# Performance work log

Hardware: AMD Instinct MI355X
Metric: run time of the kernel (lower is better)

Reference implementation:

```python
import jax, jax.numpy as jnp
import numpy as np

EPS = 1e-5

def layer_norm(x, w, b):
    mu = jnp.mean(x, axis=-1, keepdims=True)
    var = jnp.var(x, axis=-1, keepdims=True)
    return (x - mu) / jnp.sqrt(var + EPS) * w + b

def setup_inputs() -> dict:
    key = jax.random.key(0)
    B, N, C = 4, 4096, 1024
    H = 16
    MW = 4 * C
    ks = jax.random.split(key, 8)
    s = 0.02
    return {
        "x": jax.random.normal(ks[0], (B, N, C), dtype=jnp.float32),
        "ln1_w": jnp.ones((C,), jnp.float32), "ln1_b": jnp.zeros((C,), jnp.float32),
        "q_w": jax.random.normal(ks[1], (C, C), jnp.float32) * s, "q_b": jnp.zeros((C,), jnp.float32),
        "k_w": jax.random.normal(ks[2], (C, C), jnp.float32) * s, "k_b": jnp.zeros((C,), jnp.float32),
        "v_w": jax.random.normal(ks[3], (C, C), jnp.float32) * s, "v_b": jnp.zeros((C,), jnp.float32),
        "o_w": jax.random.normal(ks[4], (C, C), jnp.float32) * s, "o_b": jnp.zeros((C,), jnp.float32),
        "ln2_w": jnp.ones((C,), jnp.float32), "ln2_b": jnp.zeros((C,), jnp.float32),
        "fc_w": jax.random.normal(ks[5], (MW, C), jnp.float32) * s, "fc_b": jnp.zeros((MW,), jnp.float32),
        "proj_w": jax.random.normal(ks[6], (C, MW), jnp.float32) * s, "proj_b": jnp.zeros((C,), jnp.float32),
    }

def reference(x, ln1_w, ln1_b, q_w, q_b, k_w, k_b, v_w, v_b, o_w, o_b,
              ln2_w, ln2_b, fc_w, fc_b, proj_w, proj_b):
    B, N, C = x.shape
    H = 16
    D = C // H
    xn = layer_norm(x, ln1_w, ln1_b)
    # projections, reshape to (B, N, H, D), transpose to (B, H, N, D)
    q = (xn @ q_w.T + q_b).reshape(B, N, H, D).transpose(0, 2, 1, 3)
    k = (xn @ k_w.T + k_b).reshape(B, N, H, D).transpose(0, 2, 1, 3)
    v = (xn @ v_w.T + v_b).reshape(B, N, H, D).transpose(0, 2, 1, 3)
    # faithful to original: einsum labels treat the HEAD axis as contraction axis
    q = jax.nn.elu(q) + 1.0
    k = jax.nn.elu(k) + 1.0
    kv = jnp.einsum('bhnd,bhne->bnde', k, v)            # sum over heads -> (B,N,D,D)
    qkv = jnp.einsum('bhnd,bnde->bhne', q, kv)          # (B,H,N,D)
    k_sum = k.sum(axis=1)                               # sum over heads -> (B,N,D)
    qk = jnp.einsum('bhnd,bnd->bhn', q, k_sum)          # (B,H,N)
    attn = qkv / qk[..., None]                          # (B,H,N,D)
    attn = attn.transpose(0, 2, 1, 3).reshape(B, N, C)
    attn = attn @ o_w.T + o_b
    x = x + attn
    xn2 = layer_norm(x, ln2_w, ln2_b)
    h = jax.nn.gelu(xn2 @ fc_w.T + fc_b, approximate=False)
    x = x + (h @ proj_w.T + proj_b)
    return x
```

## Files before the change

### kernel.cpp

```cpp
#include <hip/hip_runtime.h>
#include <math.h>

typedef unsigned short u16;
typedef unsigned int   u32;
typedef __attribute__((ext_vector_type(8))) short bf16x8;
typedef __attribute__((ext_vector_type(4))) float f32x4;
typedef __attribute__((ext_vector_type(4))) unsigned short u16x4;

__device__ __forceinline__ float bf2f(u16 v){ return __uint_as_float(((u32)v) << 16); }
__device__ __forceinline__ u16 f2bf(float f){
  u32 u = __float_as_uint(f);
  return (u16)((u + 0x7fffu + ((u >> 16) & 1u)) >> 16);
}
__device__ __forceinline__ float elu1(float x){ return x > 0.f ? x + 1.f : __expf(x); }
__device__ __forceinline__ float gelu_f(float v){
  float u = 0.7978845608f * (v + 0.044715f * v * v * v);
  float e = __expf(-2.f * fabsf(u));
  float th = copysignf((1.f - e) / (1.f + e), u);
  return 0.5f * v * (1.f + th);
}

__global__ __launch_bounds__(256) void k_cast(const float* __restrict__ src, u16* __restrict__ dst, int n4){
  int i = blockIdx.x * 256 + threadIdx.x;
  int stride = gridDim.x * 256;
  for (; i < n4; i += stride){
    float4 v = ((const float4*)src)[i];
    u16x4 o; o.x = f2bf(v.x); o.y = f2bf(v.y); o.z = f2bf(v.z); o.w = f2bf(v.w);
    ((u16x4*)dst)[i] = o;
  }
}

__global__ void k_cat3(const float* __restrict__ a, const float* __restrict__ b,
                       const float* __restrict__ c, float* __restrict__ dst){
  int i = blockIdx.x * 256 + threadIdx.x;
  dst[i] = i < 1024 ? a[i] : (i < 2048 ? b[i - 1024] : c[i - 2048]);
}

__global__ __launch_bounds__(256) void k_ln(const float* __restrict__ x, const float* __restrict__ w,
                                            const float* __restrict__ b, u16* __restrict__ out){
  const int t = threadIdx.x;
  const size_t m = blockIdx.x;
  float4 v = ((const float4*)(x + m * 1024))[t];
  float s  = v.x + v.y + v.z + v.w;
  float s2 = v.x*v.x + v.y*v.y + v.z*v.z + v.w*v.w;
  #pragma unroll
  for (int o = 32; o > 0; o >>= 1){ s += __shfl_down(s, o, 64); s2 += __shfl_down(s2, o, 64); }
  __shared__ float red[8];
  if ((t & 63) == 0){ red[t >> 6] = s; red[4 + (t >> 6)] = s2; }
  __syncthreads();
  s  = red[0] + red[1] + red[2] + red[3];
  s2 = red[4] + red[5] + red[6] + red[7];
  float mu  = s * (1.f / 1024.f);
  float inv = rsqrtf(s2 * (1.f / 1024.f) - mu * mu + 1e-5f);
  float4 wv = ((const float4*)w)[t];
  float4 bv = ((const float4*)b)[t];
  u16x4 o;
  o.x = f2bf((v.x - mu) * inv * wv.x + bv.x);
  o.y = f2bf((v.y - mu) * inv * wv.y + bv.y);
  o.z = f2bf((v.z - mu) * inv * wv.z + bv.z);
  o.w = f2bf((v.w - mu) * inv * wv.w + bv.w);
  ((u16x4*)(out + m * 1024))[t] = o;
}

__global__ __launch_bounds__(256) void k_attn(const u16* __restrict__ qkv, u16* __restrict__ out){
  __shared__ float qe[4][16][68];
  __shared__ float ke[4][16][68];
  __shared__ float sm[4][16][20];
  const int w = threadIdx.x >> 6, lane = threadIdx.x & 63;
  const size_t m = (size_t)blockIdx.x * 4 + w;
  const u16* base = qkv + m * 3072;
  #pragma unroll
  for (int i = 0; i < 8; ++i){
    int idx = i * 64 + lane;
    int h = idx >> 5, c2 = (idx & 31) * 2;
    u32 qv = ((const u32*)base)[idx];
    u32 kv = ((const u32*)base)[512 + idx];
    float2 qf, kf;
    qf.x = elu1(bf2f((u16)(qv & 0xffffu))); qf.y = elu1(bf2f((u16)(qv >> 16)));
    kf.x = elu1(bf2f((u16)(kv & 0xffffu))); kf.y = elu1(bf2f((u16)(kv >> 16)));
    *(float2*)&qe[w][h][c2] = qf;
    *(float2*)&ke[w][h][c2] = kf;
  }
  float vr[16];
  #pragma unroll
  for (int h = 0; h < 16; ++h) vr[h] = bf2f(base[2048 + h * 64 + lane]);
  __syncthreads();
  const int sh = lane >> 2, jb = lane & 3;
  float sacc[4] = {0.f, 0.f, 0.f, 0.f};
  #pragma unroll
  for (int d4 = 0; d4 < 16; ++d4){
    float4 q4 = *(const float4*)&qe[w][sh][d4 * 4];
    #pragma unroll
    for (int j = 0; j < 4; ++j){
      float4 k4 = *(const float4*)&ke[w][4 * jb + j][d4 * 4];
      sacc[j] += q4.x*k4.x + q4.y*k4.y + q4.z*k4.z + q4.w*k4.w;
    }
  }
  #pragma unroll
  for (int j = 0; j < 4; ++j) sm[w][sh][4 * jb + j] = sacc[j];
  float part = sacc[0] + sacc[1] + sacc[2] + sacc[3];
  part += __shfl_xor(part, 1, 64);
  part += __shfl_xor(part, 2, 64);
  if (jb == 0) sm[w][sh][16] = part;
  __syncthreads();
  float acc[16];
  #pragma unroll
  for (int h = 0; h < 16; ++h) acc[h] = 0.f;
  #pragma unroll
  for (int h = 0; h < 16; ++h){
    #pragma unroll
    for (int j4 = 0; j4 < 4; ++j4){
      float4 s4 = *(const float4*)&sm[w][h][j4 * 4];
      acc[h] += s4.x*vr[4*j4] + s4.y*vr[4*j4+1] + s4.z*vr[4*j4+2] + s4.w*vr[4*j4+3];
    }
  }
  u16* ob = out + m * 1024;
  #pragma unroll
  for (int h = 0; h < 16; ++h)
    ob[h * 64 + lane] = f2bf(acc[h] / sm[w][h][16]);
}

template<int Q, int IB, int AE>
__device__ __forceinline__ void quadf(f32x4 (&acc)[8][4], bf16x8 (&a)[AE][2], bf16x8 (&b)[4][2]){
  __builtin_amdgcn_s_setprio(1);
  #pragma unroll
  for (int s = 0; s < 2; ++s)
    #pragma unroll
    for (int i = 0; i < 2; ++i)
      #pragma unroll
      for (int nf = 0; nf < 4; ++nf)
        acc[2*Q+i][nf] = __builtin_amdgcn_mfma_f32_16x16x32_bf16(a[IB+i][s], b[nf][s], acc[2*Q+i][nf], 0, 0, 0);
  __builtin_amdgcn_s_setprio(0);
}

template<int EPI>
__global__ __launch_bounds__(512, 2) void k_gemm(const u16* __restrict__ A, const u16* __restrict__ W,
                                                 const float* __restrict__ bias, const float* __restrict__ res,
                                                 void* __restrict__ outp, int N, int K, int nbn){
  __shared__ alignas(16) char lds[131072];
  const int tid  = threadIdx.x;
  const int lane = tid & 63, wid = tid >> 6;
  const int wr = wid >> 2, wc = wid & 3;
  const int g = lane >> 4, l15 = lane & 15;
  const int nwg = gridDim.x, bid = blockIdx.x;
  const int swz = (bid & 7) * (nwg >> 3) + (bid >> 3);
  const int m0 = (swz / nbn) * 256, n0 = (swz % nbn) * 256;
  const u16* gA = A + (size_t)m0 * K;
  const u16* gW = W + (size_t)n0 * K;
  const int nt = K >> 6;

  f32x4 acc[8][4];
  #pragma unroll
  for (int i = 0; i < 8; ++i)
    #pragma unroll
    for (int j = 0; j < 4; ++j) acc[i][j] = (f32x4){0.f, 0.f, 0.f, 0.f};

  auto stageA = [&](int b, int kt, int h){
    char* dst = lds + b * 65536 + h * 16384 + wid * 1024;
    const u16* src = gA + (size_t)(h * 128) * K + (kt << 6);
    #pragma unroll
    for (int i = 0; i < 2; ++i){
      int li = i * 512 + tid;
      int r  = li >> 3;
      int ch = (li & 7) ^ (r & 7);
      __builtin_amdgcn_global_load_lds(
        (const __attribute__((address_space(1))) u32*)(src + (size_t)r * K + ch * 8),
        (__attribute__((address_space(3))) u32*)(dst + i * 8192), 16, 0, 0);
    }
  };
  auto stageB = [&](int b, int kt, int h){
    char* dst = lds + b * 65536 + 32768 + h * 16384 + wid * 1024;
    const u16* src = gW + (size_t)(h * 128) * K + (kt << 6);
    #pragma unroll
    for (int i = 0; i < 2; ++i){
      int li = i * 512 + tid;
      int r  = li >> 3;
      int ch = (li & 7) ^ (r & 7);
      __builtin_amdgcn_global_load_lds(
        (const __attribute__((address_space(1))) u32*)(src + (size_t)r * K + ch * 8),
        (__attribute__((address_space(3))) u32*)(dst + i * 8192), 16, 0, 0);
    }
  };

  stageA(0, 0, 0); stageA(0, 0, 1); stageB(0, 0, 0); stageB(0, 0, 1);
  if (nt > 1){
    stageA(1, 1, 0); stageA(1, 1, 1);
    asm volatile("s_waitcnt vmcnt(4)" ::: "memory");
  } else {
    asm volatile("s_waitcnt vmcnt(0)" ::: "memory");
  }
  __builtin_amdgcn_s_barrier();

  for (int t = 0; t < nt; ++t){
    const int c = t & 1;
    const char* Ab = lds + c * 65536;
    const char* Bb = Ab + 32768;
    bf16x8 bfr[4][2], aQ[2][2], aH[4][2];

    #pragma unroll
    for (int nf = 0; nf < 4; ++nf)
      #pragma unroll
      for (int s = 0; s < 2; ++s){
        int row = wc * 64 + nf * 16 + l15;
        bfr[nf][s] = *(const bf16x8*)(Bb + row * 128 + (((4 * s + g) ^ (row & 7)) << 4));
      }
    #pragma unroll
    for (int i = 0; i < 2; ++i)
      #pragma unroll
      for (int s = 0; s < 2; ++s){
        int row = wr * 128 + i * 16 + l15;
        aQ[i][s] = *(const bf16x8*)(Ab + row * 128 + (((4 * s + g) ^ (row & 7)) << 4));
      }
    if (t + 1 < nt) stageB(c ^ 1, t + 1, 0);
    __builtin_amdgcn_s_barrier();
    quadf<0, 0>(acc, aQ, bfr);
    __builtin_amdgcn_s_barrier();

    #pragma unroll
    for (int i = 0; i < 2; ++i)
      #pragma unroll
      for (int s = 0; s < 2; ++s){
        int row = wr * 128 + (2 + i) * 16 + l15;
        aQ[i][s] = *(const bf16x8*)(Ab + row * 128 + (((4 * s + g) ^ (row & 7)) << 4));
      }
    #pragma unroll
    for (int i = 0; i < 4; ++i)
      #pragma unroll
      for (int s = 0; s < 2; ++s){
        int row = wr * 128 + (4 + i) * 16 + l15;
        aH[i][s] = *(const bf16x8*)(Ab + row * 128 + (((4 * s + g) ^ (row & 7)) << 4));
      }
    if (t + 1 < nt) stageB(c ^ 1, t + 1, 1);
    __builtin_amdgcn_s_barrier();
    quadf<1, 0>(acc, aQ, bfr);
    asm volatile("s_waitcnt lgkmcnt(0)" ::: "memory");
    __builtin_amdgcn_s_barrier();

    if (t + 2 < nt) stageA(c, t + 2, 0);
    __builtin_amdgcn_s_barrier();
    quadf<2, 0>(acc, aH, bfr);
    __builtin_amdgcn_s_barrier();

    if (t + 2 < nt){
      stageA(c, t + 2, 1);
      asm volatile("s_waitcnt vmcnt(4)" ::: "memory");
    } else {
      asm volatile("s_waitcnt vmcnt(0)" ::: "memory");
    }
    __builtin_amdgcn_s_barrier();
    quadf<3, 2>(acc, aH, bfr);
    __builtin_amdgcn_s_barrier();
  }

  #pragma unroll
  for (int mf = 0; mf < 8; ++mf){
    #pragma unroll
    for (int nf = 0; nf < 4; ++nf){
      int row = m0 + wr * 128 + mf * 16 + 4 * g;
      int col = n0 + wc * 64 + nf * 16 + l15;
      float bcol = bias[col];
      #pragma unroll
      for (int r = 0; r < 4; ++r){
        float v = acc[mf][nf][r] + bcol;
        size_t idx = (size_t)(row + r) * N + col;
        if constexpr (EPI == 0){
          ((u16*)outp)[idx] = f2bf(v);
        } else if constexpr (EPI == 1){
          ((float*)outp)[idx] = res[idx] + v;
        } else if constexpr (EPI == 2){
          ((u16*)outp)[idx] = f2bf(gelu_f(v));
        } else {
          float* o = (float*)outp; o[idx] = o[idx] + v;
        }
      }
    }
  }
}

extern "C" void kernel_launch(void* const* d_in, const int* in_sizes, int n_in,
                              void* d_out, int out_size, void* d_ws, size_t ws_size,
                              hipStream_t stream){
  (void)in_sizes; (void)n_in; (void)out_size; (void)ws_size;
  const float* x    = (const float*)d_in[0];
  const float* ln1w = (const float*)d_in[1];
  const float* ln1b = (const float*)d_in[2];
  const float* qw   = (const float*)d_in[3];
  const float* qb   = (const float*)d_in[4];
  const float* kw   = (const float*)d_in[5];
  const float* kb   = (const float*)d_in[6];
  const float* vw   = (const float*)d_in[7];
  const float* vb   = (const float*)d_in[8];
  const float* ow   = (const float*)d_in[9];
  const float* ob   = (const float*)d_in[10];
  const float* ln2w = (const float*)d_in[11];
  const float* ln2b = (const float*)d_in[12];
  const float* fcw  = (const float*)d_in[13];
  const float* fcb  = (const float*)d_in[14];
  const float* pw   = (const float*)d_in[15];
  const float* pb   = (const float*)d_in[16];

  char* ws = (char*)d_ws;
  u16*   WQKV = (u16*)(ws + 0);
  u16*   WO   = (u16*)(ws + 6291456);
  u16*   WFC  = (u16*)(ws + 8388608);
  u16*   WPR  = (u16*)(ws + 16777216);
  float* BQ   = (float*)(ws + 25165824);
  u16*   XN   = (u16*)(ws + 25178112);
  u16*   QKV  = (u16*)(ws + 58732544);
  u16*   ATT  = (u16*)(ws + 159395840);
  u16*   H    = QKV;
  float* OUT  = (float*)d_out;

  k_cast<<<512, 256, 0, stream>>>(qw, WQKV,           262144);
  k_cast<<<512, 256, 0, stream>>>(kw, WQKV + 1048576, 262144);
  k_cast<<<512, 256, 0, stream>>>(vw, WQKV + 2097152, 262144);
  k_cast<<<512, 256, 0, stream>>>(ow, WO,             262144);
  k_cast<<<1024, 256, 0, stream>>>(fcw, WFC,          1048576);
  k_cast<<<1024, 256, 0, stream>>>(pw,  WPR,          1048576);
  k_cat3<<<12, 256, 0, stream>>>(qb, kb, vb, BQ);

  k_ln<<<16384, 256, 0, stream>>>(x, ln1w, ln1b, XN);
  k_gemm<0><<<64 * 12, 512, 0, stream>>>(XN, WQKV, BQ, nullptr, QKV, 3072, 1024, 12);
  k_attn<<<4096, 256, 0, stream>>>(QKV, ATT);
  k_gemm<1><<<64 * 4, 512, 0, stream>>>(ATT, WO, ob, x, OUT, 1024, 1024, 4);

  k_ln<<<16384, 256, 0, stream>>>(OUT, ln2w, ln2b, XN);
  k_gemm<2><<<64 * 16, 512, 0, stream>>>(XN, WFC, fcb, nullptr, H, 4096, 1024, 16);
  k_gemm<3><<<64 * 4, 512, 0, stream>>>(H, WPR, pb, nullptr, OUT, 1024, 4096, 4);
}
```

Measured before the change: 571.6 us.

## Software-pipeline LDS fragment reads in GEMM main loop with double-buffered registers

Restructures the GEMM K-loop so each quarter's A fragments are read from LDS while the previous quarter's MFMAs run. Both A and B register fragments are now double-buffered, and the next tile's B fragments and first A quarter are prefetched before the last MFMA quarter. The loop is unrolled by two so buffer indices are compile-time constants. Barriers per iteration drop from eight to about two, which cuts synchronization stalls. The extra register buffers raise VGPR pressure at 512 threads with two blocks per CU, and the loop assumes nt is even or handled by the t+1 guards.

```diff
diff --git a/kernel.cpp b/kernel.cpp
--- a/kernel.cpp
+++ b/kernel.cpp
@@ -120,8 +120,8 @@
     ob[h * 64 + lane] = f2bf(acc[h] / sm[w][h][16]);
 }
 
-template<int Q, int IB, int AE>
-__device__ __forceinline__ void quadf(f32x4 (&acc)[8][4], bf16x8 (&a)[AE][2], bf16x8 (&b)[4][2]){
+template<int Q>
+__device__ __forceinline__ void quadf(f32x4 (&acc)[8][4], const bf16x8 (&a)[2][2], const bf16x8 (&b)[4][2]){
   __builtin_amdgcn_s_setprio(1);
   #pragma unroll
   for (int s = 0; s < 2; ++s)
@@ -129,7 +129,7 @@
     for (int i = 0; i < 2; ++i)
       #pragma unroll
       for (int nf = 0; nf < 4; ++nf)
-        acc[2*Q+i][nf] = __builtin_amdgcn_mfma_f32_16x16x32_bf16(a[IB+i][s], b[nf][s], acc[2*Q+i][nf], 0, 0, 0);
+        acc[2*Q+i][nf] = __builtin_amdgcn_mfma_f32_16x16x32_bf16(a[i][s], b[nf][s], acc[2*Q+i][nf], 0, 0, 0);
   __builtin_amdgcn_s_setprio(0);
 }
 
@@ -181,6 +181,27 @@
         (__attribute__((address_space(3))) u32*)(dst + i * 8192), 16, 0, 0);
     }
   };
+  auto rdA = [&](bf16x8 (&d)[2][2], const char* Abase, int q){
+    #pragma unroll
+    for (int i = 0; i < 2; ++i)
+      #pragma unroll
+      for (int s = 0; s < 2; ++s){
+        int row = wr * 128 + (2 * q + i) * 16 + l15;
+        d[i][s] = *(const bf16x8*)(Abase + row * 128 + (((4 * s + g) ^ (row & 7)) << 4));
+      }
+  };
+  auto rdB = [&](bf16x8 (&d)[4][2], const char* Bbase){
+    #pragma unroll
+    for (int nf = 0; nf < 4; ++nf)
+      #pragma unroll
+      for (int s = 0; s < 2; ++s){
+        int row = wc * 64 + nf * 16 + l15;
+        d[nf][s] = *(const bf16x8*)(Bbase + row * 128 + (((4 * s + g) ^ (row & 7)) << 4));
+      }
+  };
+
+  bf16x8 bfr[2][4][2];
+  bf16x8 aQ[2][2][2];
 
   stageA(0, 0, 0); stageA(0, 0, 1); stageB(0, 0, 0); stageB(0, 0, 1);
   if (nt > 1){
@@ -190,66 +211,39 @@
     asm volatile("s_waitcnt vmcnt(0)" ::: "memory");
   }
   __builtin_amdgcn_s_barrier();
-
-  for (int t = 0; t < nt; ++t){
-    const int c = t & 1;
-    const char* Ab = lds + c * 65536;
-    const char* Bb = Ab + 32768;
-    bf16x8 bfr[4][2], aQ[2][2], aH[4][2];
-
-    #pragma unroll
-    for (int nf = 0; nf < 4; ++nf)
-      #pragma unroll
-      for (int s = 0; s < 2; ++s){
-        int row = wc * 64 + nf * 16 + l15;
-        bfr[nf][s] = *(const bf16x8*)(Bb + row * 128 + (((4 * s + g) ^ (row & 7)) << 4));
-      }
-    #pragma unroll
-    for (int i = 0; i < 2; ++i)
-      #pragma unroll
-      for (int s = 0; s < 2; ++s){
-        int row = wr * 128 + i * 16 + l15;
-        aQ[i][s] = *(const bf16x8*)(Ab + row * 128 + (((4 * s + g) ^ (row & 7)) << 4));
-      }
-    if (t + 1 < nt) stageB(c ^ 1, t + 1, 0);
-    __builtin_amdgcn_s_barrier();
-    quadf<0, 0>(acc, aQ, bfr);
-    __builtin_amdgcn_s_barrier();
-
-    #pragma unroll
-    for (int i = 0; i < 2; ++i)
-      #pragma unroll
-      for (int s = 0; s < 2; ++s){
-        int row = wr * 128 + (2 + i) * 16 + l15;
-        aQ[i][s] = *(const bf16x8*)(Ab + row * 128 + (((4 * s + g) ^ (row & 7)) << 4));
-      }
-    #pragma unroll
-    for (int i = 0; i < 4; ++i)
-      #pragma unroll
-      for (int s = 0; s < 2; ++s){
-        int row = wr * 128 + (4 + i) * 16 + l15;
-        aH[i][s] = *(const bf16x8*)(Ab + row * 128 + (((4 * s + g) ^ (row & 7)) << 4));
-      }
-    if (t + 1 < nt) stageB(c ^ 1, t + 1, 1);
-    __builtin_amdgcn_s_barrier();
-    quadf<1, 0>(acc, aQ, bfr);
-    asm volatile("s_waitcnt lgkmcnt(0)" ::: "memory");
-    __builtin_amdgcn_s_barrier();
-
-    if (t + 2 < nt) stageA(c, t + 2, 0);
-    __builtin_amdgcn_s_barrier();
-    quadf<2, 0>(acc, aH, bfr);
-    __builtin_amdgcn_s_barrier();
-
-    if (t + 2 < nt){
-      stageA(c, t + 2, 1);
-      asm volatile("s_waitcnt vmcnt(4)" ::: "memory");
-    } else {
-      asm volatile("s_waitcnt vmcnt(0)" ::: "memory");
-    }
-    __builtin_amdgcn_s_barrier();
-    quadf<3, 2>(acc, aH, bfr);
-    __builtin_amdgcn_s_barrier();
+  rdB(bfr[0], lds + 32768);
+  rdA(aQ[0], lds, 0);
+
+  for (int t0 = 0; t0 < nt; t0 += 2){
+    #pragma unroll
+    for (int u = 0; u < 2; ++u){
+      const int t = t0 + u;
+      const char* Ab  = lds + u * 65536;
+      const char* Bb1 = lds + (u ^ 1) * 65536 + 32768;
+      const char* Ab1 = lds + (u ^ 1) * 65536;
+      if (t + 1 < nt) stageB(u ^ 1, t + 1, 0);
+      rdA(aQ[1], Ab, 1);
+      quadf<0>(acc, aQ[0], bfr[u]);
+      if (t + 1 < nt) stageB(u ^ 1, t + 1, 1);
+      rdA(aQ[0], Ab, 2);
+      quadf<1>(acc, aQ[1], bfr[u]);
+      rdA(aQ[1], Ab, 3);
+      quadf<2>(acc, aQ[0], bfr[u]);
+      asm volatile("s_waitcnt lgkmcnt(0)" ::: "memory");
+      __builtin_amdgcn_s_barrier();
+      if (t + 2 < nt){
+        stageA(u, t + 2, 0); stageA(u, t + 2, 1);
+        asm volatile("s_waitcnt vmcnt(4)" ::: "memory");
+      } else if (t + 1 < nt){
+        asm volatile("s_waitcnt vmcnt(0)" ::: "memory");
+      }
+      if (t + 1 < nt){
+        __builtin_amdgcn_s_barrier();
+        rdB(bfr[u ^ 1], Bb1);
+        rdA(aQ[0], Ab1, 0);
+      }
+      quadf<3>(acc, aQ[1], bfr[u]);
+    }
   }
 
   #pragma unroll
```

After: 852.7 us. +49.2%, slower.

## Restructure GEMM main loop into 4x2 MFMA quadrants with reduced register fragments

Applied to the files above, without the earlier changes.

Each k-step of the GEMM main loop now runs as four quadrants of 4 M-fragments by 2 N-fragments instead of four phases of 2 M-fragments by 4 N-fragments. LDS fragment reads are interleaved differently: B halves are loaded in two parts and A halves are reused across both B halves. Both A stagings for t+2 are issued together. The aim is to cut live register fragments and rebalance LDS reads against MFMA work, but the extra lgkmcnt waits before each quadrant may expose LDS latency.

```diff
diff --git a/kernel.cpp b/kernel.cpp
--- a/kernel.cpp
+++ b/kernel.cpp
@@ -120,16 +120,16 @@
     ob[h * 64 + lane] = f2bf(acc[h] / sm[w][h][16]);
 }
 
-template<int Q, int IB, int AE>
-__device__ __forceinline__ void quadf(f32x4 (&acc)[8][4], bf16x8 (&a)[AE][2], bf16x8 (&b)[4][2]){
+template<int QM, int QN>
+__device__ __forceinline__ void quad16(f32x4 (&acc)[8][4], const bf16x8 (&a)[4][2], const bf16x8 (&b)[2][2]){
   __builtin_amdgcn_s_setprio(1);
   #pragma unroll
   for (int s = 0; s < 2; ++s)
     #pragma unroll
-    for (int i = 0; i < 2; ++i)
+    for (int i = 0; i < 4; ++i)
       #pragma unroll
-      for (int nf = 0; nf < 4; ++nf)
-        acc[2*Q+i][nf] = __builtin_amdgcn_mfma_f32_16x16x32_bf16(a[IB+i][s], b[nf][s], acc[2*Q+i][nf], 0, 0, 0);
+      for (int j = 0; j < 2; ++j)
+        acc[QM*4+i][QN*2+j] = __builtin_amdgcn_mfma_f32_16x16x32_bf16(a[i][s], b[j][s], acc[QM*4+i][QN*2+j], 0, 0, 0);
   __builtin_amdgcn_s_setprio(0);
 }
 
@@ -181,6 +181,27 @@
         (__attribute__((address_space(3))) u32*)(dst + i * 8192), 16, 0, 0);
     }
   };
+  auto rdA4 = [&](bf16x8 (&d)[4][2], const char* Abase, int qm){
+    #pragma unroll
+    for (int i = 0; i < 4; ++i)
+      #pragma unroll
+      for (int s = 0; s < 2; ++s){
+        int row = wr * 128 + (qm * 4 + i) * 16 + l15;
+        d[i][s] = *(const bf16x8*)(Abase + row * 128 + (((4 * s + g) ^ (row & 7)) << 4));
+      }
+  };
+  auto rdB2 = [&](bf16x8 (&d)[2][2], const char* Bbase, int qn){
+    #pragma unroll
+    for (int j = 0; j < 2; ++j)
+      #pragma unroll
+      for (int s = 0; s < 2; ++s){
+        int row = wc * 64 + (qn * 2 + j) * 16 + l15;
+        d[j][s] = *(const bf16x8*)(Bbase + row * 128 + (((4 * s + g) ^ (row & 7)) << 4));
+      }
+  };
+
+  bf16x8 aA[4][2];
+  bf16x8 bB[2][2][2];
 
   stageA(0, 0, 0); stageA(0, 0, 1); stageB(0, 0, 0); stageB(0, 0, 1);
   if (nt > 1){
@@ -195,60 +216,36 @@
     const int c = t & 1;
     const char* Ab = lds + c * 65536;
     const char* Bb = Ab + 32768;
-    bf16x8 bfr[4][2], aQ[2][2], aH[4][2];
-
-    #pragma unroll
-    for (int nf = 0; nf < 4; ++nf)
-      #pragma unroll
-      for (int s = 0; s < 2; ++s){
-        int row = wc * 64 + nf * 16 + l15;
-        bfr[nf][s] = *(const bf16x8*)(Bb + row * 128 + (((4 * s + g) ^ (row & 7)) << 4));
-      }
-    #pragma unroll
-    for (int i = 0; i < 2; ++i)
-      #pragma unroll
-      for (int s = 0; s < 2; ++s){
-        int row = wr * 128 + i * 16 + l15;
-        aQ[i][s] = *(const bf16x8*)(Ab + row * 128 + (((4 * s + g) ^ (row & 7)) << 4));
-      }
+
+    rdB2(bB[0], Bb, 0);
+    rdA4(aA, Ab, 0);
     if (t + 1 < nt) stageB(c ^ 1, t + 1, 0);
     __builtin_amdgcn_s_barrier();
-    quadf<0, 0>(acc, aQ, bfr);
-    __builtin_amdgcn_s_barrier();
-
-    #pragma unroll
-    for (int i = 0; i < 2; ++i)
-      #pragma unroll
-      for (int s = 0; s < 2; ++s){
-        int row = wr * 128 + (2 + i) * 16 + l15;
-        aQ[i][s] = *(const bf16x8*)(Ab + row * 128 + (((4 * s + g) ^ (row & 7)) << 4));
-      }
-    #pragma unroll
-    for (int i = 0; i < 4; ++i)
-      #pragma unroll
-      for (int s = 0; s < 2; ++s){
-        int row = wr * 128 + (4 + i) * 16 + l15;
-        aH[i][s] = *(const bf16x8*)(Ab + row * 128 + (((4 * s + g) ^ (row & 7)) << 4));
-      }
+    asm volatile("s_waitcnt lgkmcnt(0)" ::: "memory");
+    quad16<0, 0>(acc, aA, bB[0]);
+    __builtin_amdgcn_s_barrier();
+
+    rdB2(bB[1], Bb, 1);
     if (t + 1 < nt) stageB(c ^ 1, t + 1, 1);
     __builtin_amdgcn_s_barrier();
-    quadf<1, 0>(acc, aQ, bfr);
     asm volatile("s_waitcnt lgkmcnt(0)" ::: "memory");
-    __builtin_amdgcn_s_barrier();
-
-    if (t + 2 < nt) stageA(c, t + 2, 0);
-    __builtin_amdgcn_s_barrier();
-    quadf<2, 0>(acc, aH, bfr);
-    __builtin_amdgcn_s_barrier();
-
+    quad16<0, 1>(acc, aA, bB[1]);
+    __builtin_amdgcn_s_barrier();
+
+    rdA4(aA, Ab, 1);
+    __builtin_amdgcn_s_barrier();
+    asm volatile("s_waitcnt lgkmcnt(0)" ::: "memory");
+    quad16<1, 0>(acc, aA, bB[0]);
+    __builtin_amdgcn_s_barrier();
+
+    if (t + 2 < nt){ stageA(c, t + 2, 0); stageA(c, t + 2, 1); }
+    __builtin_amdgcn_s_barrier();
+    quad16<1, 1>(acc, aA, bB[1]);
     if (t + 2 < nt){
-      stageA(c, t + 2, 1);
       asm volatile("s_waitcnt vmcnt(4)" ::: "memory");
     } else {
       asm volatile("s_waitcnt vmcnt(0)" ::: "memory");
     }
-    __builtin_amdgcn_s_barrier();
-    quadf<3, 2>(acc, aH, bfr);
     __builtin_amdgcn_s_barrier();
   }
 
```

New measurement: 580.6 us. About the same (+1.6%).
